# Performance work log

Measured on AMD Instinct MI355X. Metric: run time of the kernel, lower is better.

## Reference

```python
import jax, jax.numpy as jnp
import numpy as np

KERNEL_SIZES = (2, 3, 4, 5)
B, T = 128, 512
CH, EMB, CHID, HID = 128, 64, 128, 256


def conv1d_same(x, w, b):
    # x: [B, T, Cin], w: [K, Cin, Cout] -> [B, T, Cout]
    y = jax.lax.conv_general_dilated(
        x, w, window_strides=(1,), padding='SAME',
        dimension_numbers=('NWC', 'WIO', 'NWC'))
    return y + b


def gru_last_state(x, Wx, Wh, b_in, b_rec):
    # Keras GRU v2 (reset_after=True), gate order z, r, h. x: [B, T, C].
    H = Wh.shape[0]
    xw = jnp.einsum('btc,ch->bth', x, Wx) + b_in  # precompute input projections [B,T,3H]

    def step(h, xt):
        hw = h @ Wh + b_rec
        xz, xr, xh = jnp.split(xt, 3, axis=-1)
        hz, hr, hh = jnp.split(hw, 3, axis=-1)
        z = jax.nn.sigmoid(xz + hz)
        r = jax.nn.sigmoid(xr + hr)
        hc = jnp.tanh(xh + r * hh)
        return z * h + (1.0 - z) * hc, None

    h0 = jnp.zeros((x.shape[0], H), x.dtype)
    hT, _ = jax.lax.scan(step, h0, jnp.swapaxes(xw, 0, 1))  # scan over time
    return hT  # [B, H]


def setup_inputs() -> dict:
    key = jax.random.key(0)
    ks = jax.random.split(key, 16)
    inp = {}
    inp['X'] = jax.random.randint(ks[0], (B, T), 0, CH)
    inp['emb_table'] = jax.random.normal(ks[1], (CH, EMB), jnp.float32) * 0.05
    s_conv = 1.0 / np.sqrt(EMB)
    for i, k in enumerate(KERNEL_SIZES):
        inp[f'conv_w{k}'] = jax.random.normal(ks[2 + i], (k, EMB, CHID), jnp.float32) * s_conv
        inp[f'conv_b{k}'] = jnp.zeros((CHID,), jnp.float32)
    cin = CHID * len(KERNEL_SIZES)
    inp['gru_Wx'] = jax.random.normal(ks[10], (cin, 3 * HID), jnp.float32) * (1.0 / np.sqrt(cin))
    inp['gru_Wh'] = jax.random.normal(ks[11], (HID, 3 * HID), jnp.float32) * (1.0 / np.sqrt(HID))
    inp['gru_b_in'] = jnp.zeros((3 * HID,), jnp.float32)
    inp['gru_b_rec'] = jnp.zeros((3 * HID,), jnp.float32)
    return inp


def reference(X, emb_table, conv_w2, conv_b2, conv_w3, conv_b3, conv_w4, conv_b4,
              conv_w5, conv_b5, gru_Wx, gru_Wh, gru_b_in, gru_b_rec):
    xe = emb_table[X]  # [B, T, EMB]
    convs = [conv1d_same(xe, w, b) for (w, b) in
             ((conv_w2, conv_b2), (conv_w3, conv_b3), (conv_w4, conv_b4), (conv_w5, conv_b5))]
    xcat = jnp.concatenate(convs, axis=-1)  # [B, T, 4*CHID]
    return gru_last_state(xcat, gru_Wx, gru_Wh, gru_b_in, gru_b_rec)  # [B, HID]
```

## Files before the change

### kernel.cpp

```cpp
#include <hip/hip_runtime.h>
#include <hip/hip_bf16.h>


typedef float f32x4 __attribute__((ext_vector_type(4)));
typedef short s16x8 __attribute__((ext_vector_type(8)));
typedef int   i32x4 __attribute__((ext_vector_type(4)));
typedef unsigned short u16;
typedef unsigned int   u32;
typedef unsigned long long u64;

#define OFF_WC    0u
#define OFF_EMBW  983040u
#define OFF_BEFF  2949120u
#define OFF_WHP   2952192u
#define OFF_MODE  3345408u
#define OFF_HGP   3345472u
#define WS_NEED   3607616u

__device__ __forceinline__ float bf2f(u16 v){
  unsigned u = ((unsigned)v) << 16; return __builtin_bit_cast(float, u);
}
__device__ __forceinline__ u16 f2bf(float f){
  unsigned u = __builtin_bit_cast(unsigned, f);
  unsigned r = u + 0x7FFFu + ((u >> 16) & 1u);
  return (u16)(r >> 16);
}
__device__ __forceinline__ float ldv(const void* p, int i, int m){
  return m ? ((const float*)p)[i] : bf2f(((const u16*)p)[i]);
}

__global__ void k_init(char* ws){
  int idx = blockIdx.x*256 + threadIdx.x;
  u32* hg = (u32*)(ws + OFF_HGP);
  if (idx < 65536) hg[idx] = 0u;
}

__global__ void k_probe(const void* __restrict__ emb, char* ws){
  const u16* w = (const u16*)emb;
  const int ln = threadIdx.x;
  bool bad = false;
  for (int j = 0; j < 8; ++j){
    u16 v = w[ln*8 + j];
    if (((v >> 7) & 0xFF) >= 0x86) bad = true;
  }
  unsigned long long m = __ballot(bad);
  if (ln == 0) *(int*)(ws + OFF_MODE) = (__popcll(m) > 4) ? 1 : 0;
}

__global__ void k_wc(const void* __restrict__ w2, const void* __restrict__ w3,
                     const void* __restrict__ w4, const void* __restrict__ w5,
                     const void* __restrict__ Wx, char* ws){
  const int md = *(const int*)(ws + OFF_MODE);
  const int d = blockIdx.x >> 6;
  const int e = blockIdx.x & 63;
  const int j0 = threadIdx.x;
  const void* wv[4] = {w2,w3,w4,w5};
  const int Kk[4] = {2,3,4,5}, pd[4] = {0,1,1,2};
  float a0=0.f, a1=0.f, a2=0.f;
  for (int br=0; br<4; ++br){
    int k = d - 2 + pd[br];
    if (k < 0 || k >= Kk[br]) continue;
    const int wbase  = (k*64 + e)*128;
    const int wxbase = (br*128)*768;
    for (int c=0; c<128; ++c){
      float wcv = ldv(wv[br], wbase + c, md);
      a0 += wcv * ldv(Wx, wxbase + c*768 + j0      , md);
      a1 += wcv * ldv(Wx, wxbase + c*768 + j0 + 256, md);
      a2 += wcv * ldv(Wx, wxbase + c*768 + j0 + 512, md);
    }
  }
  float* o = (float*)(ws + OFF_WC) + (d*64 + e)*768;
  o[j0] = a0; o[j0+256] = a1; o[j0+512] = a2;
}

__global__ void k_beff(const void* __restrict__ b2, const void* __restrict__ b3,
                       const void* __restrict__ b4, const void* __restrict__ b5,
                       const void* __restrict__ Wx, const void* __restrict__ bin,
                       char* ws){
  const int md = *(const int*)(ws + OFF_MODE);
  int j = blockIdx.x*256 + threadIdx.x;
  if (j >= 768) return;
  const void* bv[4] = {b2,b3,b4,b5};
  float acc = ldv(bin, j, md);
  for (int br=0; br<4; ++br)
    for (int c=0; c<128; ++c)
      acc += ldv(bv[br], c, md) * ldv(Wx, (br*128 + c)*768 + j, md);
  ((float*)(ws + OFF_BEFF))[j] = acc;
}

__global__ void k_embw(const void* __restrict__ emb, char* ws){
  const int md = *(const int*)(ws + OFF_MODE);
  const int d = blockIdx.x >> 7, ch = blockIdx.x & 127;
  const float* wc = (const float*)(ws + OFF_WC) + d*64*768;
  float* ew = (float*)(ws + OFF_EMBW) + (size_t)(d*128 + ch)*768;
  const int j0 = threadIdx.x;
  float a0=0.f, a1=0.f, a2=0.f;
  for (int e=0; e<64; ++e){
    float ev = ldv(emb, ch*64 + e, md);
    a0 += ev*wc[e*768 + j0      ];
    a1 += ev*wc[e*768 + j0 + 256];
    a2 += ev*wc[e*768 + j0 + 512];
  }
  ew[j0] = a0; ew[j0+256] = a1; ew[j0+512] = a2;
}

__global__ void k_whp(const void* __restrict__ Wh, char* ws){
  const int md = *(const int*)(ws + OFF_MODE);
  const int j = blockIdx.x, k = threadIdx.x;
  ((u16*)(ws + OFF_WHP))[j*256 + k] = f2bf(ldv(Wh, k*768 + j, md));
}

__launch_bounds__(512, 1)
__global__ void k_gru(const int* __restrict__ X, const void* __restrict__ brec,
                      char* __restrict__ ws, void* __restrict__ outv){
  const int tid = threadIdx.x;
  const int w   = tid >> 6, ln = tid & 63;
  const int l15 = ln & 15, l4 = ln >> 4;
  const int g = blockIdx.x >> 2, r = blockIdx.x & 3;

  const int md = *(const int*)(ws + OFF_MODE);
  const float* embw = (const float*)(ws + OFF_EMBW);
  const float* beff = (const float*)(ws + OFF_BEFF);
  const u16*   whp  = (const u16*)(ws + OFF_WHP);
  u32* hgp = (u32*)(ws + OFF_HGP);

  __shared__ int   Xs[16*512];
  __shared__ float xwlds[2][16][196];
  __shared__ float hwp[2][16][196];
  __shared__ u16   hstage[2][16][272];

  for (int i = tid; i < 2048; i += 512)
    ((i32x4*)Xs)[i] = ((const i32x4*)(X + g*16*512))[i];

  const int qs = (w >> 2) * 4;
  s16x8 Bf[3][4];
  #pragma unroll
  for (int gg=0; gg<3; ++gg){
    const int col = gg*256 + r*64 + (w&3)*16 + l15;
    #pragma unroll
    for (int qi=0; qi<4; ++qi)
      Bf[gg][qi] = *(const s16x8*)(whp + col*256 + (qs+qi)*32 + l4*8);
  }

  const int c63 = tid & 63;
  const int tr  = (tid >> 6) & 7;
  const int hc  = r*64 + c63;
  const float br0 = ldv(brec,       hc, md);
  const float br1 = ldv(brec, 256 + hc, md);
  const float br2 = ldv(brec, 512 + hc, md);

  const int row1 = tid / 48,      rem1 = tid % 48;
  const int gg1  = rem1 / 16,     cc1  = rem1 % 16;
  const int cid2 = tid + 512;
  const int row2 = cid2 / 48,     rem2 = cid2 % 48;
  const int gg2  = rem2 / 16,     cc2  = rem2 % 16;
  const bool two = (tid < 256);
  const int gcol1 = gg1*256 + r*64 + cc1*4;
  const int gcol2 = gg2*256 + r*64 + cc2*4;
  const f32x4 be1 = *(const f32x4*)(beff + gcol1);
  const f32x4 be2 = *(const f32x4*)(beff + gcol2);

  const int srow = tid >> 5, sc0_ = (tid & 31) * 8;

  __syncthreads();

  {
    f32x4 v1 = be1, v2 = be2;
    #pragma unroll
    for (int d=0; d<5; ++d){
      const int t = d - 2;
      if ((unsigned)t < 512u){
        const int ch1 = Xs[row1*512 + t] & 127;
        v1 += *(const f32x4*)(embw + (size_t)(d*128 + ch1)*768 + gcol1);
        if (two){
          const int ch2 = Xs[row2*512 + t] & 127;
          v2 += *(const f32x4*)(embw + (size_t)(d*128 + ch2)*768 + gcol2);
        }
      }
    }
    *(f32x4*)&xwlds[0][row1][gg1*64 + cc1*4] = v1;
    if (two) *(f32x4*)&xwlds[0][row2][gg2*64 + cc2*4] = v2;
  }
  float hpA = 0.f, hpB = 0.f;
  __syncthreads();

  for (int s = 0; s < 512; ++s){
    const int par = s & 1;

    const u32 em = (u32)((s >> 1) & 1);
    const u32* hb = hgp + (unsigned)par*32768u + (unsigned)g*4096u
                    + (unsigned)srow*256u + (unsigned)sc0_;
    i32x4 A, B;
    {
      int guard = 0;
      for (;;){
        asm volatile("global_load_dwordx4 %0, %2, off sc0 sc1\n\t"
                     "global_load_dwordx4 %1, %3, off sc0 sc1"
                     : "=&v"(A), "=&v"(B)
                     : "v"(hb), "v"(hb + 4)
                     : "memory");
        asm volatile("s_waitcnt vmcnt(0)" : "+v"(A), "+v"(B) :: "memory");
        __builtin_amdgcn_sched_barrier(0);
        const u32 ba = (u32)A[0] & (u32)A[1] & (u32)A[2] & (u32)A[3]
                     & (u32)B[0] & (u32)B[1] & (u32)B[2] & (u32)B[3];
        const u32 bo = (u32)A[0] | (u32)A[1] | (u32)A[2] | (u32)A[3]
                     | (u32)B[0] | (u32)B[1] | (u32)B[2] | (u32)B[3];
        const bool ok = em ? ((ba & 1u) == 1u) : ((bo & 1u) == 0u);
        if (ok || ++guard > (1<<20)) break;
      }
    }
    {
      u32 wd[8] = {(u32)A[0],(u32)A[1],(u32)A[2],(u32)A[3],
                   (u32)B[0],(u32)B[1],(u32)B[2],(u32)B[3]};
      s16x8 hi, lo;
      #pragma unroll
      for (int j=0; j<8; ++j){ hi[j] = (short)(wd[j] >> 16); lo[j] = (short)(wd[j] & 0xFFFFu); }
      *(s16x8*)&hstage[0][srow][sc0_] = hi;
      *(s16x8*)&hstage[1][srow][sc0_] = lo;
    }
    __syncthreads();

    f32x4 a0 = {0.f,0.f,0.f,0.f}, a1 = a0, a2 = a0;
    #pragma unroll
    for (int qi=0; qi<4; ++qi){
      const int kb = (qs+qi)*32 + l4*8;
      const s16x8 ahi = *(const s16x8*)&hstage[0][l15][kb];
      const s16x8 alo = *(const s16x8*)&hstage[1][l15][kb];
      a0 = __builtin_amdgcn_mfma_f32_16x16x32_bf16(ahi, Bf[0][qi], a0, 0,0,0);
      a1 = __builtin_amdgcn_mfma_f32_16x16x32_bf16(ahi, Bf[1][qi], a1, 0,0,0);
      a2 = __builtin_amdgcn_mfma_f32_16x16x32_bf16(ahi, Bf[2][qi], a2, 0,0,0);
      a0 = __builtin_amdgcn_mfma_f32_16x16x32_bf16(alo, Bf[0][qi], a0, 0,0,0);
      a1 = __builtin_amdgcn_mfma_f32_16x16x32_bf16(alo, Bf[1][qi], a1, 0,0,0);
      a2 = __builtin_amdgcn_mfma_f32_16x16x32_bf16(alo, Bf[2][qi], a2, 0,0,0);
    }
    {
      const int kh = w >> 2, sc = (w&3)*16 + l15;
      #pragma unroll
      for (int p=0; p<4; ++p){
        hwp[kh][l4*4+p][       sc] = a0[p];
        hwp[kh][l4*4+p][ 64 + sc] = a1[p];
        hwp[kh][l4*4+p][128 + sc] = a2[p];
      }
    }

    f32x4 n1, n2;
    if (s < 511){
      n1 = be1; n2 = be2;
      #pragma unroll
      for (int d=0; d<5; ++d){
        const int t = s - 1 + d;
        if ((unsigned)t < 512u){
          const int ch1 = Xs[row1*512 + t] & 127;
          n1 += *(const f32x4*)(embw + (size_t)(d*128 + ch1)*768 + gcol1);
          if (two){
            const int ch2 = Xs[row2*512 + t] & 127;
            n2 += *(const f32x4*)(embw + (size_t)(d*128 + ch2)*768 + gcol2);
          }
        }
      }
    }
    __syncthreads();

    float hnA, hnB;
    #pragma unroll
    for (int u=0; u<2; ++u){
      const int row = tr + u*8;
      const float hz = hwp[0][row][      c63] + hwp[1][row][      c63] + br0;
      const float hr = hwp[0][row][ 64 + c63] + hwp[1][row][ 64 + c63] + br1;
      const float hh = hwp[0][row][128 + c63] + hwp[1][row][128 + c63] + br2;
      const float xz = xwlds[par][row][      c63];
      const float xr = xwlds[par][row][ 64 + c63];
      const float xh = xwlds[par][row][128 + c63];
      const float hp = u ? hpB : hpA;
      const float z  = 1.f/(1.f + __expf(-(xz + hz)));
      const float rg = 1.f/(1.f + __expf(-(xr + hr)));
      const float pre = xh + rg*hh;
      const float e2  = __expf(-2.f*fabsf(pre));
      const float th  = __builtin_copysignf((1.f - e2)/(1.f + e2), pre);
      const float hn  = z*hp + (1.f - z)*th;
      if (u) hnB = hn; else hnA = hn;
    }
    hpA = hnA; hpB = hnB;

    if (s == 511){
      const int i0 = (g*16 + tr)*256 + hc;
      if (md){ ((float*)outv)[i0] = hnA; ((float*)outv)[i0 + 8*256] = hnB; }
      else   { ((u16*)outv)[i0] = f2bf(hnA); ((u16*)outv)[i0 + 8*256] = f2bf(hnB); }
    } else {
      const u32 sm = (u32)(((s + 1) >> 1) & 1);
      u32* hb2 = hgp + (unsigned)(par^1)*32768u + (unsigned)g*4096u;
      #pragma unroll
      for (int u=0; u<2; ++u){
        const float hn = u ? hnB : hnA;
        const u32 bh = f2bf(hn);
        u32 bl = f2bf(hn - bf2f((u16)bh));
        bl = (bl & ~1u) | sm;
        __hip_atomic_store(hb2 + (tr + u*8)*256 + hc, (bh << 16) | bl,
                           __ATOMIC_RELAXED, __HIP_MEMORY_SCOPE_AGENT);
      }
      *(f32x4*)&xwlds[par^1][row1][gg1*64 + cc1*4] = n1;
      if (two) *(f32x4*)&xwlds[par^1][row2][gg2*64 + cc2*4] = n2;
    }
  }
}

extern "C" void kernel_launch(void* const* d_in, const int* in_sizes, int n_in,
                              void* d_out, int out_size, void* d_ws, size_t ws_size,
                              hipStream_t stream){
  const int* X = (const int*)d_in[0];
  char* ws = (char*)d_ws;
  if (ws_size < WS_NEED) return;

  k_init <<<256, 256, 0, stream>>>(ws);
  k_probe<<<  1,  64, 0, stream>>>(d_in[1], ws);
  k_wc   <<<320, 256, 0, stream>>>(d_in[2], d_in[4], d_in[6], d_in[8], d_in[10], ws);
  k_beff <<<  3, 256, 0, stream>>>(d_in[3], d_in[5], d_in[7], d_in[9], d_in[10], d_in[12], ws);
  k_embw <<<640, 256, 0, stream>>>(d_in[1], ws);
  k_whp  <<<768, 256, 0, stream>>>(d_in[11], ws);
  k_gru  <<< 32, 512, 0, stream>>>(X, d_in[13], ws, d_out);
}
```

Before: 2.010 ms.

## Assign GRU groups to blocks by XCC and exchange hidden state via L2 atomics

At startup each block reads its hardware XCC id and takes a dynamic (group, rank) assignment so that the four blocks sharing one batch group land on the same XCD where possible. A handshake checks whether L2-scoped atomics are coherent among those blocks. If it passes, the per-step hidden-state exchange uses global_atomic_swap for publishing and global_atomic_or reads with the sc0 bit only, instead of sc0 sc1 system-coherent loads. The goal is to keep the 512-step recurrence synchronisation inside the local L2 rather than going through the slower device-wide coherence path. The cost is a startup grid barrier, eight scalar atomics per poll instead of two vector loads, and a dependence on all 32 blocks being co-resident.

Measured after the change: 4.152 ms. 107% more time.

```diff
diff --git a/kernel.cpp b/kernel.cpp
--- a/kernel.cpp
+++ b/kernel.cpp
@@ -15,7 +15,11 @@
 #define OFF_WHP   2952192u
 #define OFF_MODE  3345408u
 #define OFF_HGP   3345472u
-#define WS_NEED   3607616u
+#define OFF_CTL   3607616u
+#define WS_NEED   3609024u
+
+#define MAGIC1 0xA5A5A5A5u
+#define MAGIC2 0x5A5A5A5Au
 
 __device__ __forceinline__ float bf2f(u16 v){
   unsigned u = ((unsigned)v) << 16; return __builtin_bit_cast(float, u);
@@ -28,11 +32,22 @@
 __device__ __forceinline__ float ldv(const void* p, int i, int m){
   return m ? ((const float*)p)[i] : bf2f(((const u16*)p)[i]);
 }
+__device__ __forceinline__ u32 atom_read(u32* p){
+  u32 rv, z = 0u;
+  asm volatile("global_atomic_or %0, %1, %2, off sc0"
+               : "=&v"(rv) : "v"(p), "v"(z) : "memory");
+  asm volatile("s_waitcnt vmcnt(0)" : "+v"(rv) :: "memory");
+  return rv;
+}
+__device__ __forceinline__ void atom_pub(u32* p, u32 v){
+  asm volatile("global_atomic_swap %0, %1, off" :: "v"(p), "v"(v) : "memory");
+}
 
 __global__ void k_init(char* ws){
   int idx = blockIdx.x*256 + threadIdx.x;
   u32* hg = (u32*)(ws + OFF_HGP);
   if (idx < 65536) hg[idx] = 0u;
+  if (idx < 352) ((u32*)(ws + OFF_CTL))[idx] = 0u;
 }
 
 __global__ void k_probe(const void* __restrict__ emb, char* ws){
@@ -116,7 +131,6 @@
   const int tid = threadIdx.x;
   const int w   = tid >> 6, ln = tid & 63;
   const int l15 = ln & 15, l4 = ln >> 4;
-  const int g = blockIdx.x >> 2, r = blockIdx.x & 3;
 
   const int md = *(const int*)(ws + OFF_MODE);
   const float* embw = (const float*)(ws + OFF_EMBW);
@@ -128,6 +142,69 @@
   __shared__ float xwlds[2][16][196];
   __shared__ float hwp[2][16][196];
   __shared__ u16   hstage[2][16][272];
+  __shared__ int   blkinfo[3];
+
+  if (tid == 0){
+    int xcc = 0;
+    asm volatile("s_getreg_b32 %0, hwreg(HW_REG_XCC_ID)" : "=s"(xcc));
+    xcc &= 7;
+    int* ctl = (int*)(ws + OFF_CTL);
+    int rank = __hip_atomic_fetch_add(&ctl[xcc], 1, __ATOMIC_RELAXED, __HIP_MEMORY_SCOPE_AGENT);
+    __hip_atomic_fetch_add(&ctl[8], 1, __ATOMIC_RELEASE, __HIP_MEMORY_SCOPE_AGENT);
+    int guard = 0;
+    while (__hip_atomic_load(&ctl[8], __ATOMIC_ACQUIRE, __HIP_MEMORY_SCOPE_AGENT) < 32){
+      if (++guard > (1<<24)) break;
+    }
+    int cnt[8];
+    #pragma unroll
+    for (int x=0; x<8; ++x)
+      cnt[x] = __hip_atomic_load(&ctl[x], __ATOMIC_RELAXED, __HIP_MEMORY_SCOPE_AGENT);
+    int g_, r_;
+    if (rank < 4){ g_ = xcc; r_ = rank; }
+    else {
+      int oidx = rank - 4;
+      for (int x=0; x<xcc; ++x){ int e = cnt[x]-4; if (e>0) oidx += e; }
+      g_ = 0; r_ = 0; int k = 0;
+      for (int x=0; x<8; ++x){
+        int have = cnt[x] < 4 ? cnt[x] : 4;
+        for (int rr=have; rr<4; ++rr){ if (k == oidx){ g_ = x; r_ = rr; } ++k; }
+      }
+    }
+    int local_final = 0;
+    if (cnt[g_] >= 4 && rank < 4){
+      u32* tw   = (u32*)(ws + OFF_CTL + 128u*(1u + (unsigned)g_));
+      int* vcnt  = (int*)(ws + OFF_CTL + 128u*9u);
+      int* vcnt2 = (int*)(ws + OFF_CTL + 128u*10u);
+      if (r_ == 0) atom_pub(tw, MAGIC1);
+      int saw1 = 0;
+      for (int t = 0; t < (1<<14); ++t){
+        if (atom_read(tw) == MAGIC1){ saw1 = 1; break; }
+      }
+      __hip_atomic_fetch_add(&vcnt2[g_], 1, __ATOMIC_RELEASE, __HIP_MEMORY_SCOPE_AGENT);
+      if (r_ == 0){
+        guard = 0;
+        while (__hip_atomic_load(&vcnt2[g_], __ATOMIC_ACQUIRE, __HIP_MEMORY_SCOPE_AGENT) < 4){
+          if (++guard > (1<<22)) break;
+        }
+        atom_pub(tw, MAGIC2);
+      }
+      int saw2 = 0;
+      for (int t = 0; t < (1<<14); ++t){
+        if (atom_read(tw) == MAGIC2){ saw2 = 1; break; }
+      }
+      __hip_atomic_fetch_add(&vcnt[g_], (saw1 && saw2) ? 1 : 16, __ATOMIC_RELEASE, __HIP_MEMORY_SCOPE_AGENT);
+      int vg = 0; guard = 0;
+      for (;;){
+        vg = __hip_atomic_load(&vcnt[g_], __ATOMIC_ACQUIRE, __HIP_MEMORY_SCOPE_AGENT);
+        if (vg >= 4 || ++guard > (1<<22)) break;
+      }
+      local_final = (vg == 4) ? 1 : 0;
+    }
+    blkinfo[0] = g_; blkinfo[1] = r_; blkinfo[2] = local_final;
+  }
+  __syncthreads();
+  const int g = blkinfo[0], r = blkinfo[1];
+  const bool localg = blkinfo[2] != 0;
 
   for (int i = tid; i < 2048; i += 512)
     ((i32x4*)Xs)[i] = ((const i32x4*)(X + g*16*512))[i];
@@ -188,16 +265,47 @@
     const int par = s & 1;
 
     const u32 em = (u32)((s >> 1) & 1);
-    const u32* hb = hgp + (unsigned)par*32768u + (unsigned)g*4096u
-                    + (unsigned)srow*256u + (unsigned)sc0_;
-    i32x4 A, B;
-    {
+    u32* hb = hgp + (unsigned)par*32768u + (unsigned)g*4096u
+              + (unsigned)srow*256u + (unsigned)sc0_;
+    u32 wd[8];
+    if (localg){
+      u32 z = 0u;
+      int guard = 0;
+      for (;;){
+        u32 w0,w1,w2,w3,w4,w5,w6,w7;
+        asm volatile(
+          "global_atomic_or %0, %8, %9, off sc0\n\t"
+          "global_atomic_or %1, %8, %9, off offset:4 sc0\n\t"
+          "global_atomic_or %2, %8, %9, off offset:8 sc0\n\t"
+          "global_atomic_or %3, %8, %9, off offset:12 sc0\n\t"
+          "global_atomic_or %4, %8, %9, off offset:16 sc0\n\t"
+          "global_atomic_or %5, %8, %9, off offset:20 sc0\n\t"
+          "global_atomic_or %6, %8, %9, off offset:24 sc0\n\t"
+          "global_atomic_or %7, %8, %9, off offset:28 sc0"
+          : "=&v"(w0),"=&v"(w1),"=&v"(w2),"=&v"(w3),
+            "=&v"(w4),"=&v"(w5),"=&v"(w6),"=&v"(w7)
+          : "v"(hb), "v"(z)
+          : "memory");
+        asm volatile("s_waitcnt vmcnt(0)"
+          : "+v"(w0),"+v"(w1),"+v"(w2),"+v"(w3),
+            "+v"(w4),"+v"(w5),"+v"(w6),"+v"(w7) :: "memory");
+        __builtin_amdgcn_sched_barrier(0);
+        wd[0]=w0; wd[1]=w1; wd[2]=w2; wd[3]=w3;
+        wd[4]=w4; wd[5]=w5; wd[6]=w6; wd[7]=w7;
+        u32 ba = ~0u, bo = 0u;
+        #pragma unroll
+        for (int j=0; j<8; ++j){ ba &= wd[j]; bo |= wd[j]; }
+        const bool ok = em ? ((ba & 1u) == 1u) : ((bo & 1u) == 0u);
+        if (ok || ++guard > (1<<18)) break;
+      }
+    } else {
+      i32x4 A, B;
       int guard = 0;
       for (;;){
         asm volatile("global_load_dwordx4 %0, %2, off sc0 sc1\n\t"
                      "global_load_dwordx4 %1, %3, off sc0 sc1"
                      : "=&v"(A), "=&v"(B)
-                     : "v"(hb), "v"(hb + 4)
+                     : "v"((const u32*)hb), "v"((const u32*)hb + 4)
                      : "memory");
         asm volatile("s_waitcnt vmcnt(0)" : "+v"(A), "+v"(B) :: "memory");
         __builtin_amdgcn_sched_barrier(0);
@@ -208,10 +316,10 @@
         const bool ok = em ? ((ba & 1u) == 1u) : ((bo & 1u) == 0u);
         if (ok || ++guard > (1<<20)) break;
       }
+      wd[0]=(u32)A[0]; wd[1]=(u32)A[1]; wd[2]=(u32)A[2]; wd[3]=(u32)A[3];
+      wd[4]=(u32)B[0]; wd[5]=(u32)B[1]; wd[6]=(u32)B[2]; wd[7]=(u32)B[3];
     }
     {
-      u32 wd[8] = {(u32)A[0],(u32)A[1],(u32)A[2],(u32)A[3],
-                   (u32)B[0],(u32)B[1],(u32)B[2],(u32)B[3]};
       s16x8 hi, lo;
       #pragma unroll
       for (int j=0; j<8; ++j){ hi[j] = (short)(wd[j] >> 16); lo[j] = (short)(wd[j] & 0xFFFFu); }
@@ -295,8 +403,12 @@
         const u32 bh = f2bf(hn);
         u32 bl = f2bf(hn - bf2f((u16)bh));
         bl = (bl & ~1u) | sm;
-        __hip_atomic_store(hb2 + (tr + u*8)*256 + hc, (bh << 16) | bl,
-                           __ATOMIC_RELAXED, __HIP_MEMORY_SCOPE_AGENT);
+        const u32 word = (bh << 16) | bl;
+        u32* dst = hb2 + (tr + u*8)*256 + hc;
+        if (localg)
+          atom_pub(dst, word);
+        else
+          __hip_atomic_store(dst, word, __ATOMIC_RELAXED, __HIP_MEMORY_SCOPE_AGENT);
       }
       *(f32x4*)&xwlds[par^1][row1][gg1*64 + cc1*4] = n1;
       if (two) *(f32x4*)&xwlds[par^1][row2][gg2*64 + cc2*4] = n2;
```

## Interleave two batch groups per GRU block to overlap cross-block sync

Applied to the files above, without the earlier changes.

Each GRU block now processes two 16-row batch groups in alternation, so the launch shrinks from 32 to 16 blocks. The goal is to hide the cross-block hidden-state handshake latency of one group behind the matmul and gate work of the other. The shared-memory copy of X is removed and token ids are read from global memory each step. The second parity buffer is now initialized to 1, which stops step 1 from accepting a buffer that has not been written yet. In exchange, each block does twice the serial work per step and loses some parallelism across CUs.

Result: slower. 3.614 ms (+79.8%).

```diff
diff --git a/kernel.cpp b/kernel.cpp
--- a/kernel.cpp
+++ b/kernel.cpp
@@ -32,7 +32,7 @@
 __global__ void k_init(char* ws){
   int idx = blockIdx.x*256 + threadIdx.x;
   u32* hg = (u32*)(ws + OFF_HGP);
-  if (idx < 65536) hg[idx] = 0u;
+  if (idx < 65536) hg[idx] = (idx < 32768) ? 0u : 1u;
 }
 
 __global__ void k_probe(const void* __restrict__ emb, char* ws){
@@ -116,7 +116,8 @@
   const int tid = threadIdx.x;
   const int w   = tid >> 6, ln = tid & 63;
   const int l15 = ln & 15, l4 = ln >> 4;
-  const int g = blockIdx.x >> 2, r = blockIdx.x & 3;
+  const int pr = blockIdx.x >> 2, r = blockIdx.x & 3;
+  const int g0 = pr*2;
 
   const int md = *(const int*)(ws + OFF_MODE);
   const float* embw = (const float*)(ws + OFF_EMBW);
@@ -124,13 +125,9 @@
   const u16*   whp  = (const u16*)(ws + OFF_WHP);
   u32* hgp = (u32*)(ws + OFF_HGP);
 
-  __shared__ int   Xs[16*512];
-  __shared__ float xwlds[2][16][196];
+  __shared__ float xwlds[2][2][16][196];
   __shared__ float hwp[2][16][196];
   __shared__ u16   hstage[2][16][272];
-
-  for (int i = tid; i < 2048; i += 512)
-    ((i32x4*)Xs)[i] = ((const i32x4*)(X + g*16*512))[i];
 
   const int qs = (w >> 2) * 4;
   s16x8 Bf[3][4];
@@ -157,149 +154,155 @@
   const bool two = (tid < 256);
   const int gcol1 = gg1*256 + r*64 + cc1*4;
   const int gcol2 = gg2*256 + r*64 + cc2*4;
+  const int o1 = gg1*64 + cc1*4, o2 = gg2*64 + cc2*4;
   const f32x4 be1 = *(const f32x4*)(beff + gcol1);
   const f32x4 be2 = *(const f32x4*)(beff + gcol2);
 
   const int srow = tid >> 5, sc0_ = (tid & 31) * 8;
 
-  __syncthreads();
-
-  {
+  #pragma unroll
+  for (int st=0; st<2; ++st){
+    const int g = g0 + st;
     f32x4 v1 = be1, v2 = be2;
     #pragma unroll
     for (int d=0; d<5; ++d){
       const int t = d - 2;
       if ((unsigned)t < 512u){
-        const int ch1 = Xs[row1*512 + t] & 127;
+        const int ch1 = X[(g*16 + row1)*512 + t] & 127;
         v1 += *(const f32x4*)(embw + (size_t)(d*128 + ch1)*768 + gcol1);
         if (two){
-          const int ch2 = Xs[row2*512 + t] & 127;
+          const int ch2 = X[(g*16 + row2)*512 + t] & 127;
           v2 += *(const f32x4*)(embw + (size_t)(d*128 + ch2)*768 + gcol2);
         }
       }
     }
-    *(f32x4*)&xwlds[0][row1][gg1*64 + cc1*4] = v1;
-    if (two) *(f32x4*)&xwlds[0][row2][gg2*64 + cc2*4] = v2;
-  }
-  float hpA = 0.f, hpB = 0.f;
+    *(f32x4*)&xwlds[st][0][row1][o1] = v1;
+    if (two) *(f32x4*)&xwlds[st][0][row2][o2] = v2;
+  }
+  float hp[2][2] = {{0.f,0.f},{0.f,0.f}};
   __syncthreads();
 
   for (int s = 0; s < 512; ++s){
     const int par = s & 1;
-
     const u32 em = (u32)((s >> 1) & 1);
-    const u32* hb = hgp + (unsigned)par*32768u + (unsigned)g*4096u
-                    + (unsigned)srow*256u + (unsigned)sc0_;
-    i32x4 A, B;
-    {
-      int guard = 0;
-      for (;;){
-        asm volatile("global_load_dwordx4 %0, %2, off sc0 sc1\n\t"
-                     "global_load_dwordx4 %1, %3, off sc0 sc1"
-                     : "=&v"(A), "=&v"(B)
-                     : "v"(hb), "v"(hb + 4)
-                     : "memory");
-        asm volatile("s_waitcnt vmcnt(0)" : "+v"(A), "+v"(B) :: "memory");
-        __builtin_amdgcn_sched_barrier(0);
-        const u32 ba = (u32)A[0] & (u32)A[1] & (u32)A[2] & (u32)A[3]
-                     & (u32)B[0] & (u32)B[1] & (u32)B[2] & (u32)B[3];
-        const u32 bo = (u32)A[0] | (u32)A[1] | (u32)A[2] | (u32)A[3]
-                     | (u32)B[0] | (u32)B[1] | (u32)B[2] | (u32)B[3];
-        const bool ok = em ? ((ba & 1u) == 1u) : ((bo & 1u) == 0u);
-        if (ok || ++guard > (1<<20)) break;
-      }
-    }
-    {
-      u32 wd[8] = {(u32)A[0],(u32)A[1],(u32)A[2],(u32)A[3],
-                   (u32)B[0],(u32)B[1],(u32)B[2],(u32)B[3]};
-      s16x8 hi, lo;
+    const u32 sm = (u32)(((s + 1) >> 1) & 1);
+
+    #pragma unroll
+    for (int st=0; st<2; ++st){
+      const int g = g0 + st;
+
+      u32* hb = hgp + (unsigned)par*32768u + (unsigned)g*4096u
+                + (unsigned)srow*256u + (unsigned)sc0_;
+      i32x4 A, B;
+      {
+        int guard = 0;
+        for (;;){
+          asm volatile("global_load_dwordx4 %0, %2, off sc0 sc1\n\t"
+                       "global_load_dwordx4 %1, %3, off sc0 sc1"
+                       : "=&v"(A), "=&v"(B)
+                       : "v"((const u32*)hb), "v"((const u32*)hb + 4)
+                       : "memory");
+          asm volatile("s_waitcnt vmcnt(0)" : "+v"(A), "+v"(B) :: "memory");
+          __builtin_amdgcn_sched_barrier(0);
+          const u32 ba = (u32)A[0] & (u32)A[1] & (u32)A[2] & (u32)A[3]
+                       & (u32)B[0] & (u32)B[1] & (u32)B[2] & (u32)B[3];
+          const u32 bo = (u32)A[0] | (u32)A[1] | (u32)A[2] | (u32)A[3]
+                       | (u32)B[0] | (u32)B[1] | (u32)B[2] | (u32)B[3];
+          const bool ok = em ? ((ba & 1u) == 1u) : ((bo & 1u) == 0u);
+          if (ok || ++guard > (1<<16)) break;
+        }
+      }
+      {
+        u32 wd[8] = {(u32)A[0],(u32)A[1],(u32)A[2],(u32)A[3],
+                     (u32)B[0],(u32)B[1],(u32)B[2],(u32)B[3]};
+        s16x8 hi, lo;
+        #pragma unroll
+        for (int j=0; j<8; ++j){ hi[j] = (short)(wd[j] >> 16); lo[j] = (short)(wd[j] & 0xFFFFu); }
+        *(s16x8*)&hstage[0][srow][sc0_] = hi;
+        *(s16x8*)&hstage[1][srow][sc0_] = lo;
+      }
+      __syncthreads();
+
+      f32x4 a0 = {0.f,0.f,0.f,0.f}, a1 = a0, a2 = a0;
       #pragma unroll
-      for (int j=0; j<8; ++j){ hi[j] = (short)(wd[j] >> 16); lo[j] = (short)(wd[j] & 0xFFFFu); }
-      *(s16x8*)&hstage[0][srow][sc0_] = hi;
-      *(s16x8*)&hstage[1][srow][sc0_] = lo;
-    }
-    __syncthreads();
-
-    f32x4 a0 = {0.f,0.f,0.f,0.f}, a1 = a0, a2 = a0;
-    #pragma unroll
-    for (int qi=0; qi<4; ++qi){
-      const int kb = (qs+qi)*32 + l4*8;
-      const s16x8 ahi = *(const s16x8*)&hstage[0][l15][kb];
-      const s16x8 alo = *(const s16x8*)&hstage[1][l15][kb];
-      a0 = __builtin_amdgcn_mfma_f32_16x16x32_bf16(ahi, Bf[0][qi], a0, 0,0,0);
-      a1 = __builtin_amdgcn_mfma_f32_16x16x32_bf16(ahi, Bf[1][qi], a1, 0,0,0);
-      a2 = __builtin_amdgcn_mfma_f32_16x16x32_bf16(ahi, Bf[2][qi], a2, 0,0,0);
-      a0 = __builtin_amdgcn_mfma_f32_16x16x32_bf16(alo, Bf[0][qi], a0, 0,0,0);
-      a1 = __builtin_amdgcn_mfma_f32_16x16x32_bf16(alo, Bf[1][qi], a1, 0,0,0);
-      a2 = __builtin_amdgcn_mfma_f32_16x16x32_bf16(alo, Bf[2][qi], a2, 0,0,0);
-    }
-    {
-      const int kh = w >> 2, sc = (w&3)*16 + l15;
-      #pragma unroll
-      for (int p=0; p<4; ++p){
-        hwp[kh][l4*4+p][       sc] = a0[p];
-        hwp[kh][l4*4+p][ 64 + sc] = a1[p];
-        hwp[kh][l4*4+p][128 + sc] = a2[p];
-      }
-    }
-
-    f32x4 n1, n2;
-    if (s < 511){
-      n1 = be1; n2 = be2;
-      #pragma unroll
-      for (int d=0; d<5; ++d){
-        const int t = s - 1 + d;
-        if ((unsigned)t < 512u){
-          const int ch1 = Xs[row1*512 + t] & 127;
-          n1 += *(const f32x4*)(embw + (size_t)(d*128 + ch1)*768 + gcol1);
-          if (two){
-            const int ch2 = Xs[row2*512 + t] & 127;
-            n2 += *(const f32x4*)(embw + (size_t)(d*128 + ch2)*768 + gcol2);
+      for (int qi=0; qi<4; ++qi){
+        const int kb = (qs+qi)*32 + l4*8;
+        const s16x8 ahi = *(const s16x8*)&hstage[0][l15][kb];
+        const s16x8 alo = *(const s16x8*)&hstage[1][l15][kb];
+        a0 = __builtin_amdgcn_mfma_f32_16x16x32_bf16(ahi, Bf[0][qi], a0, 0,0,0);
+        a1 = __builtin_amdgcn_mfma_f32_16x16x32_bf16(ahi, Bf[1][qi], a1, 0,0,0);
+        a2 = __builtin_amdgcn_mfma_f32_16x16x32_bf16(ahi, Bf[2][qi], a2, 0,0,0);
+        a0 = __builtin_amdgcn_mfma_f32_16x16x32_bf16(alo, Bf[0][qi], a0, 0,0,0);
+        a1 = __builtin_amdgcn_mfma_f32_16x16x32_bf16(alo, Bf[1][qi], a1, 0,0,0);
+        a2 = __builtin_amdgcn_mfma_f32_16x16x32_bf16(alo, Bf[2][qi], a2, 0,0,0);
+      }
+      {
+        const int kh = w >> 2, sc = (w&3)*16 + l15;
+        #pragma unroll
+        for (int p=0; p<4; ++p){
+          hwp[kh][l4*4+p][       sc] = a0[p];
+          hwp[kh][l4*4+p][ 64 + sc] = a1[p];
+          hwp[kh][l4*4+p][128 + sc] = a2[p];
+        }
+      }
+
+      f32x4 n1, n2;
+      if (s < 511){
+        n1 = be1; n2 = be2;
+        #pragma unroll
+        for (int d=0; d<5; ++d){
+          const int t = s - 1 + d;
+          if ((unsigned)t < 512u){
+            const int ch1 = X[(g*16 + row1)*512 + t] & 127;
+            n1 += *(const f32x4*)(embw + (size_t)(d*128 + ch1)*768 + gcol1);
+            if (two){
+              const int ch2 = X[(g*16 + row2)*512 + t] & 127;
+              n2 += *(const f32x4*)(embw + (size_t)(d*128 + ch2)*768 + gcol2);
+            }
           }
         }
       }
-    }
-    __syncthreads();
-
-    float hnA, hnB;
-    #pragma unroll
-    for (int u=0; u<2; ++u){
-      const int row = tr + u*8;
-      const float hz = hwp[0][row][      c63] + hwp[1][row][      c63] + br0;
-      const float hr = hwp[0][row][ 64 + c63] + hwp[1][row][ 64 + c63] + br1;
-      const float hh = hwp[0][row][128 + c63] + hwp[1][row][128 + c63] + br2;
-      const float xz = xwlds[par][row][      c63];
-      const float xr = xwlds[par][row][ 64 + c63];
-      const float xh = xwlds[par][row][128 + c63];
-      const float hp = u ? hpB : hpA;
-      const float z  = 1.f/(1.f + __expf(-(xz + hz)));
-      const float rg = 1.f/(1.f + __expf(-(xr + hr)));
-      const float pre = xh + rg*hh;
-      const float e2  = __expf(-2.f*fabsf(pre));
-      const float th  = __builtin_copysignf((1.f - e2)/(1.f + e2), pre);
-      const float hn  = z*hp + (1.f - z)*th;
-      if (u) hnB = hn; else hnA = hn;
-    }
-    hpA = hnA; hpB = hnB;
-
-    if (s == 511){
-      const int i0 = (g*16 + tr)*256 + hc;
-      if (md){ ((float*)outv)[i0] = hnA; ((float*)outv)[i0 + 8*256] = hnB; }
-      else   { ((u16*)outv)[i0] = f2bf(hnA); ((u16*)outv)[i0 + 8*256] = f2bf(hnB); }
-    } else {
-      const u32 sm = (u32)(((s + 1) >> 1) & 1);
-      u32* hb2 = hgp + (unsigned)(par^1)*32768u + (unsigned)g*4096u;
+      __syncthreads();
+
+      float hnA, hnB;
       #pragma unroll
       for (int u=0; u<2; ++u){
-        const float hn = u ? hnB : hnA;
-        const u32 bh = f2bf(hn);
-        u32 bl = f2bf(hn - bf2f((u16)bh));
-        bl = (bl & ~1u) | sm;
-        __hip_atomic_store(hb2 + (tr + u*8)*256 + hc, (bh << 16) | bl,
-                           __ATOMIC_RELAXED, __HIP_MEMORY_SCOPE_AGENT);
-      }
-      *(f32x4*)&xwlds[par^1][row1][gg1*64 + cc1*4] = n1;
-      if (two) *(f32x4*)&xwlds[par^1][row2][gg2*64 + cc2*4] = n2;
+        const int row = tr + u*8;
+        const float hz = hwp[0][row][      c63] + hwp[1][row][      c63] + br0;
+        const float hr = hwp[0][row][ 64 + c63] + hwp[1][row][ 64 + c63] + br1;
+        const float hh = hwp[0][row][128 + c63] + hwp[1][row][128 + c63] + br2;
+        const float xz = xwlds[st][par][row][      c63];
+        const float xr = xwlds[st][par][row][ 64 + c63];
+        const float xh = xwlds[st][par][row][128 + c63];
+        const float hpv = hp[st][u];
+        const float z  = 1.f/(1.f + __expf(-(xz + hz)));
+        const float rg = 1.f/(1.f + __expf(-(xr + hr)));
+        const float pre = xh + rg*hh;
+        const float e2  = __expf(-2.f*fabsf(pre));
+        const float th  = __builtin_copysignf((1.f - e2)/(1.f + e2), pre);
+        const float hn  = z*hpv + (1.f - z)*th;
+        if (u) hnB = hn; else hnA = hn;
+      }
+      hp[st][0] = hnA; hp[st][1] = hnB;
+
+      if (s == 511){
+        const int i0 = (g*16 + tr)*256 + hc;
+        if (md){ ((float*)outv)[i0] = hnA; ((float*)outv)[i0 + 8*256] = hnB; }
+        else   { ((u16*)outv)[i0] = f2bf(hnA); ((u16*)outv)[i0 + 8*256] = f2bf(hnB); }
+      } else {
+        u32* hb2 = hgp + (unsigned)(par^1)*32768u + (unsigned)g*4096u;
+        #pragma unroll
+        for (int u=0; u<2; ++u){
+          const float hn = u ? hnB : hnA;
+          const u32 bh = f2bf(hn);
+          u32 bl = f2bf(hn - bf2f((u16)bh));
+          bl = (bl & ~1u) | sm;
+          __hip_atomic_store(hb2 + (tr + u*8)*256 + hc, (bh << 16) | bl,
+                             __ATOMIC_RELAXED, __HIP_MEMORY_SCOPE_AGENT);
+        }
+        *(f32x4*)&xwlds[st][par^1][row1][o1] = n1;
+        if (two) *(f32x4*)&xwlds[st][par^1][row2][o2] = n2;
+      }
     }
   }
 }
@@ -317,5 +320,5 @@
   k_beff <<<  3, 256, 0, stream>>>(d_in[3], d_in[5], d_in[7], d_in[9], d_in[10], d_in[12], ws);
   k_embw <<<640, 256, 0, stream>>>(d_in[1], ws);
   k_whp  <<<768, 256, 0, stream>>>(d_in[11], ws);
-  k_gru  <<< 32, 512, 0, stream>>>(X, d_in[13], ws, d_out);
-}
+  k_gru  <<< 16, 512, 0, stream>>>(X, d_in[13], ws, d_out);
+}
```
